# Kernel tuning notes

Measured on AMD Instinct MI355X. Metric: run time of the kernel, lower is better.

The kernel has to match this reference:

```python
import jax, jax.numpy as jnp
import numpy as np

INPUT_DIM = 246
HIDDEN = 512
OUTPUT_DIM = 123
B, T = 128, 500
N_DIFF, N_ABIL = 11, 8


def setup_inputs() -> dict:
    key = jax.random.key(0)
    ks = jax.random.split(key, 9)
    feats = jax.random.normal(ks[0], (B, T, INPUT_DIM), dtype=jnp.float32)
    ability = jax.random.randint(ks[1], (B, T, 1), 0, N_ABIL).astype(jnp.float32)
    diff = jax.random.randint(ks[2], (B, T, 1), 0, N_DIFF).astype(jnp.float32)
    x = jnp.concatenate([feats, ability, diff], axis=-1)  # [B,T,248]
    in_dim = INPUT_DIM + N_DIFF + N_ABIL  # 265
    s_ih = 1.0 / np.sqrt(HIDDEN)
    W_ih = jax.random.uniform(ks[3], (4 * HIDDEN, in_dim), jnp.float32, -s_ih, s_ih)
    W_hh = jax.random.uniform(ks[4], (4 * HIDDEN, HIDDEN), jnp.float32, -s_ih, s_ih)
    b_ih = jax.random.uniform(ks[5], (4 * HIDDEN,), jnp.float32, -s_ih, s_ih)
    b_hh = jax.random.uniform(ks[6], (4 * HIDDEN,), jnp.float32, -s_ih, s_ih)
    s_fc = 1.0 / np.sqrt(HIDDEN)
    W_fc = jax.random.uniform(ks[7], (OUTPUT_DIM, HIDDEN), jnp.float32, -s_fc, s_fc)
    b_fc = jax.random.uniform(ks[8], (OUTPUT_DIM,), jnp.float32, -s_fc, s_fc)
    return {"x": x, "W_ih": W_ih, "W_hh": W_hh, "b_ih": b_ih, "b_hh": b_hh,
            "W_fc": W_fc, "b_fc": b_fc}


def _lstm(x, W_ih, W_hh, b_ih, b_hh):
    # x: [B,T,In] -> out: [B,T,H]; PyTorch gate order i,f,g,o
    Bsz = x.shape[0]
    H = W_hh.shape[1]
    x_proj = jnp.einsum('bti,gi->btg', x, W_ih) + b_ih + b_hh  # [B,T,4H]

    def step(carry, xt):
        h, c = carry
        gates = xt + h @ W_hh.T
        i, f, g, o = jnp.split(gates, 4, axis=-1)
        i, f, o = jax.nn.sigmoid(i), jax.nn.sigmoid(f), jax.nn.sigmoid(o)
        g = jnp.tanh(g)
        c = f * c + i * g
        h = o * jnp.tanh(c)
        return (h, c), h

    h0 = jnp.zeros((Bsz, H), x.dtype)
    c0 = jnp.zeros((Bsz, H), x.dtype)
    (_, _), hs = jax.lax.scan(step, (h0, c0), x_proj.transpose(1, 0, 2))
    return hs.transpose(1, 0, 2)


def reference(x, W_ih, W_hh, b_ih, b_hh, W_fc, b_fc):
    feats = x[..., :INPUT_DIM]
    ability = x[..., -2].astype(jnp.int32)
    diff = x[..., -1].astype(jnp.int32)
    one_hot_diff = jax.nn.one_hot(diff, N_DIFF, dtype=x.dtype)
    one_hot_ab = jax.nn.one_hot(ability, N_ABIL, dtype=x.dtype)
    new_x = jnp.tanh(jnp.concatenate([feats, one_hot_diff, one_hot_ab], axis=-1))
    out = _lstm(new_x, W_ih, W_hh, b_ih, b_hh)  # [B,T,H]
    res = jax.nn.sigmoid(jnp.einsum('bth,oh->bto', out, W_fc) + b_fc)
    return res[:, :-1, :]
```

## Files before the change

kernel.cpp:

```cpp
#include <hip/hip_runtime.h>
#include <hip/hip_fp16.h>


typedef _Float16 f16;
typedef _Float16 f16x8 __attribute__((ext_vector_type(8)));
typedef float f32x4 __attribute__((ext_vector_type(4)));
typedef unsigned u32x4 __attribute__((ext_vector_type(4)));

#define TS 499

#define NEWX_OFF   0ul
#define NEWX_BYTES (500ul*8*9216)
#define HALL_OFF   (NEWX_OFF + NEWX_BYTES)
#define HALL_BYTES (500ul*128*512*2)
#define WHH_OFF    (HALL_OFF + HALL_BYTES)
#define WHH_BYTES  (2048ul*512*2)
#define WIH_OFF    (WHH_OFF + WHH_BYTES)
#define WIH_BYTES  (2048ul*288*2)
#define WFC_OFF    (WIH_OFF + WIH_BYTES)
#define WFC_BYTES  (128ul*512*2)
#define BIAS_OFF   (WFC_OFF + WFC_BYTES)
#define BIAS_BYTES (2048ul*4)
#define WS_NEED    (BIAS_OFF + BIAS_BYTES)

__device__ __forceinline__ float tanh_dev(float x) {
    float ax = fabsf(x);
    float e  = __expf(-2.f * ax);
    float r  = (1.f - e) / (1.f + e);
    return copysignf(r, x);
}
__device__ __forceinline__ float sigm_dev(float x) {
    float e = __expf(-fabsf(x));
    float p = 1.f / (1.f + e);
    return x >= 0.f ? p : 1.f - p;
}

__global__ void __launch_bounds__(256) prep_newx(const float* __restrict__ x,
                                                 f16* __restrict__ newx) {
    const int t  = blockIdx.x;
    const int bt = blockIdx.y;
    const int tid = threadIdx.x;
    char* tb = (char*)newx + ((size_t)t * 8 + bt) * 9216;
    for (int idx = tid; idx < 16 * 288; idx += 256) {
        const int r = idx / 288, k = idx - r * 288;
        const float* xr = x + ((size_t)(bt * 16 + r) * 500 + t) * 248;
        float v;
        if (k < 246)      v = tanh_dev(xr[k]);
        else if (k < 257) v = (k - 246 == (int)xr[247]) ? 0.76159415595576485f : 0.f;
        else if (k < 265) v = (k - 257 == (int)xr[246]) ? 0.76159415595576485f : 0.f;
        else              v = 0.f;
        const int col8 = k >> 3;
        const int byte = (col8 >> 2) * 1024 + (((col8 & 3) * 16 + r) << 4) + ((k & 7) << 1);
        *(f16*)(tb + byte) = (f16)v;
    }
}

__global__ void __launch_bounds__(256) prep_w(const float* __restrict__ W_ih,
                                              const float* __restrict__ W_hh,
                                              const float* __restrict__ W_fc,
                                              const float* __restrict__ b_ih,
                                              const float* __restrict__ b_hh,
                                              f16* __restrict__ whh, f16* __restrict__ wih,
                                              f16* __restrict__ wfc, float* __restrict__ bias) {
    const int NHH = 2048 * 512;
    const int NIH = 2048 * 288;
    const int NFC = 128 * 512;
    const int NT  = NHH + NIH + NFC + 2048;
    for (int i = blockIdx.x * 256 + threadIdx.x; i < NT; i += gridDim.x * 256) {
        if (i < NHH) {
            whh[i] = (f16)W_hh[i];
        } else if (i < NHH + NIH) {
            int j2 = i - NHH; int rr = j2 / 288, kk = j2 % 288;
            wih[j2] = (kk < 265) ? (f16)W_ih[rr * 265 + kk] : (f16)0.f;
        } else if (i < NHH + NIH + NFC) {
            int j2 = i - (NHH + NIH); int rr = j2 >> 9, kk = j2 & 511;
            wfc[j2] = (rr < 123) ? (f16)W_fc[rr * 512 + kk] : (f16)0.f;
        } else {
            int j2 = i - (NHH + NIH + NFC);
            bias[j2] = b_ih[j2] + b_hh[j2];
        }
    }
}

#define CHKU16(H) { u32x4 _u = __builtin_bit_cast(u32x4, H);                  \
    bad |= (unsigned)((_u[0] >> 16) == 0xFFFFu) | (unsigned)((_u[0] & 0xFFFFu) == 0xFFFFu); \
    bad |= (unsigned)((_u[1] >> 16) == 0xFFFFu) | (unsigned)((_u[1] & 0xFFFFu) == 0xFFFFu); \
    bad |= (unsigned)((_u[2] >> 16) == 0xFFFFu) | (unsigned)((_u[2] & 0xFFFFu) == 0xFFFFu); \
    bad |= (unsigned)((_u[3] >> 16) == 0xFFFFu) | (unsigned)((_u[3] & 0xFFFFu) == 0xFFFFu); }

__device__ __forceinline__ u32x4 scrub(u32x4 h) {
    u32x4 u = h;
    #pragma unroll
    for (int i = 0; i < 4; ++i) {
        unsigned v = u[i];
        if ((v & 0xFFFFu) == 0xFFFFu) v &= 0xFFFF0000u;
        if ((v >> 16)     == 0xFFFFu) v &= 0x0000FFFFu;
        u[i] = v;
    }
    return u;
}

__global__ void __launch_bounds__(512, 1) lstm_seq(const f16* __restrict__ newx_,
                                                   f16* __restrict__ hall,
                                                   const f16* __restrict__ whh,
                                                   const f16* __restrict__ wih,
                                                   const float* __restrict__ bias) {
    __shared__ __align__(16) char hsb[16 * 1024];
    __shared__ float gf[4 * 560];
    __shared__ __align__(16) f16 hout[512];

    const char* newx = (const char*)newx_;
    const int tid = threadIdx.x, bid = blockIdx.x;
    const int btile = bid & 7;
    const int hsl   = bid >> 3;

    const int w = tid >> 6, wl = tid & 63;
    const int arow = wl & 15, kgrp = wl >> 4;
    const int g = w & 3, cb = w >> 2;
    const int grow = g * 512 + hsl * 32 + cb * 16 + arow;
    const int bE = tid >> 5, colE = tid & 31;

    f16x8 wh[16], wi[9];
    #pragma unroll
    for (int kc = 0; kc < 16; ++kc)
        wh[kc] = *(const f16x8*)(whh + (size_t)grow * 512 + kc * 32 + kgrp * 8);
    #pragma unroll
    for (int kc = 0; kc < 9; ++kc)
        wi[kc] = *(const f16x8*)(wih + (size_t)grow * 288 + kc * 32 + kgrp * 8);
    const float bb = bias[grow];

    const int srow = tid & 15, sc8 = tid >> 4;
    const int soff1 = (sc8 >> 2) * 1024 + (((sc8 & 3) * 16 + srow) << 4);
    const int soff2 = soff1 + 8 * 1024;

    float c_st = 0.f;

    f16x8 xa[9];
    {
        const char* xt = newx + (size_t)btile * 9216;
        #pragma unroll
        for (int kc = 0; kc < 9; ++kc)
            xa[kc] = *(const f16x8*)(xt + kc * 1024 + wl * 16);
    }

    for (int t = 0; t < TS; ++t) {
        f32x4 acc = {bb, bb, bb, bb};
        #pragma unroll
        for (int kc = 0; kc < 9; ++kc)
            acc = __builtin_amdgcn_mfma_f32_16x16x32_f16(xa[kc], wi[kc], acc, 0, 0, 0);
        {
            const char* xt1 = newx + ((size_t)(t + 1) * 8 + btile) * 9216;
            #pragma unroll
            for (int kc = 0; kc < 9; ++kc)
                xa[kc] = *(const f16x8*)(xt1 + kc * 1024 + wl * 16);
        }

        if (t > 0) {
            const char* hb = (const char*)hall + ((size_t)(t - 1) * 128 + btile * 16) * 1024;
            const char* ga1 = hb + srow * 1024 + sc8 * 16;
            const char* ga2 = ga1 + 512;
            u32x4 h0, h1;
            int spins = 0;
            bool timeout = false;
            for (;;) {
                asm volatile("global_load_dwordx4 %0, %2, off sc0 sc1\n\t"
                             "global_load_dwordx4 %1, %3, off sc0 sc1\n\t"
                             "s_waitcnt vmcnt(0)"
                             : "=&v"(h0), "=&v"(h1) : "v"(ga1), "v"(ga2) : "memory");
                unsigned bad = 0;
                CHKU16(h0); CHKU16(h1);
                if (__ballot(bad) == 0ull) break;
                if (++spins > 4096) { timeout = true; break; }
                if (spins > 2) __builtin_amdgcn_s_sleep(4);
            }
            if (timeout) { h0 = scrub(h0); h1 = scrub(h1); }
            *(u32x4*)(hsb + soff1) = h0;
            *(u32x4*)(hsb + soff2) = h1;
            __syncthreads();

            f32x4 e0 = {0.f,0.f,0.f,0.f}, e1 = {0.f,0.f,0.f,0.f};
            #pragma unroll
            for (int kc = 0; kc < 16; kc += 2) {
                f16x8 a0 = *(const f16x8*)(hsb + kc * 1024 + wl * 16);
                f16x8 a1 = *(const f16x8*)(hsb + (kc + 1) * 1024 + wl * 16);
                e0 = __builtin_amdgcn_mfma_f32_16x16x32_f16(a0, wh[kc],     e0, 0, 0, 0);
                e1 = __builtin_amdgcn_mfma_f32_16x16x32_f16(a1, wh[kc + 1], e1, 0, 0, 0);
            }
            acc += e0; acc += e1;
        }

        {
            float* gp = gf + g * 560 + cb * 16 + (wl & 15);
            const int b4 = (wl >> 4) * 4;
            gp[(b4 + 0) * 35] = acc[0];
            gp[(b4 + 1) * 35] = acc[1];
            gp[(b4 + 2) * 35] = acc[2];
            gp[(b4 + 3) * 35] = acc[3];
        }
        __syncthreads();

        {
            const float* gq = gf + bE * 35 + colE;
            float iv = sigm_dev(gq[0]);
            float fv = sigm_dev(gq[560]);
            float gv = tanh_dev(gq[1120]);
            float ov = sigm_dev(gq[1680]);
            c_st = fv * c_st + iv * gv;
            float hv = ov * tanh_dev(c_st);
            hout[bE * 32 + colE] = (f16)hv;
        }
        __syncthreads();

        if ((tid >> 6) == (t & 7)) {
            u32x4 hv4 = *(const u32x4*)((const char*)hout + wl * 16);
            const f16* sp = hall + ((size_t)t * 128 + btile * 16 + (wl >> 2)) * 512
                            + hsl * 32 + (wl & 3) * 8;
            asm volatile("global_store_dwordx4 %0, %1, off sc0 sc1"
                         :: "v"(sp), "v"(hv4) : "memory");
        }
    }
}

__global__ void __launch_bounds__(256) out_gemm(const f16* __restrict__ hall,
                                                const f16* __restrict__ wfc,
                                                const float* __restrict__ bfc,
                                                float* __restrict__ out) {
    const int tid = threadIdx.x;
    const int w = tid >> 6, wl = tid & 63;
    const int arow = wl & 15, kgrp = wl >> 4;
    const long m0 = (long)blockIdx.x * 64 + w * 16;
    const f16* ap = hall + (m0 + arow) * 512 + kgrp * 8;
    f16x8 a[16];
    #pragma unroll
    for (int kc = 0; kc < 16; ++kc) a[kc] = *(const f16x8*)(ap + kc * 32);
    #pragma unroll
    for (int jt = 0; jt < 8; ++jt) {
        f32x4 acc = {0.f, 0.f, 0.f, 0.f};
        const f16* bp = wfc + (size_t)(jt * 16 + arow) * 512 + kgrp * 8;
        #pragma unroll
        for (int kc = 0; kc < 16; ++kc)
            acc = __builtin_amdgcn_mfma_f32_16x16x32_f16(a[kc], *(const f16x8*)(bp + kc * 32),
                                                         acc, 0, 0, 0);
        const int col = jt * 16 + arow;
        if (col < 123) {
            const float bv = bfc[col];
            #pragma unroll
            for (int rr = 0; rr < 4; ++rr) {
                long m = m0 + kgrp * 4 + rr;
                int tt = (int)(m >> 7), b = (int)(m & 127);
                out[((size_t)b * 499 + tt) * 123 + col] = sigm_dev(acc[rr] + bv);
            }
        }
    }
}

extern "C" void kernel_launch(void* const* d_in, const int* in_sizes, int n_in,
                              void* d_out, int out_size, void* d_ws, size_t ws_size,
                              hipStream_t stream) {
    if (ws_size < WS_NEED) return;

    const float* x    = (const float*)d_in[0];
    const float* W_ih = (const float*)d_in[1];
    const float* W_hh = (const float*)d_in[2];
    const float* b_ih = (const float*)d_in[3];
    const float* b_hh = (const float*)d_in[4];
    const float* W_fc = (const float*)d_in[5];
    const float* b_fc = (const float*)d_in[6];
    float* out = (float*)d_out;
    char* ws = (char*)d_ws;

    f16* newx   = (f16*)(ws + NEWX_OFF);
    f16* hall   = (f16*)(ws + HALL_OFF);
    f16* whh    = (f16*)(ws + WHH_OFF);
    f16* wih    = (f16*)(ws + WIH_OFF);
    f16* wfc    = (f16*)(ws + WFC_OFF);
    float* bias = (float*)(ws + BIAS_OFF);

    (void)hipMemsetAsync(hall, 0xFF, HALL_BYTES, stream);

    prep_newx<<<dim3(TS, 8), 256, 0, stream>>>(x, newx);
    prep_w<<<512, 256, 0, stream>>>(W_ih, W_hh, W_fc, b_ih, b_hh, whh, wih, wfc, bias);

    lstm_seq<<<dim3(128), dim3(512), 0, stream>>>(newx, hall, whh, wih, bias);

    out_gemm<<<998, 256, 0, stream>>>(hall, wfc, b_fc, out);
}
```

Measured before the change: 1.260 ms.

## Give each wave all four gates so the LSTM cell update stays in registers

The persistent LSTM kernel now runs 64 blocks of 256 threads instead of 128 blocks of 512. Each wave computes the i, f, g and o gates for its own 16 hidden columns, so the cell update runs directly on the MFMA accumulators. This drops the shared-memory gate exchange and one barrier per step, and fewer blocks take part in the cross-block spin-wait on h. In exchange each wave does four times the recurrent MFMA work and holds 64 fragments of W_hh in registers. W_ih is no longer kept in registers and is re-read from global memory every step, which adds load latency on the serial critical path.

```diff
diff --git a/kernel.cpp b/kernel.cpp
--- a/kernel.cpp
+++ b/kernel.cpp
@@ -100,40 +100,45 @@
     return u;
 }
 
-__global__ void __launch_bounds__(512, 1) lstm_seq(const f16* __restrict__ newx_,
+#define MFMA16(A, B, C) __builtin_amdgcn_mfma_f32_16x16x32_f16(A, B, C, 0, 0, 0)
+
+__global__ void __launch_bounds__(256, 1) lstm_seq(const f16* __restrict__ newx_,
                                                    f16* __restrict__ hall,
                                                    const f16* __restrict__ whh,
                                                    const f16* __restrict__ wih,
                                                    const float* __restrict__ bias) {
     __shared__ __align__(16) char hsb[16 * 1024];
-    __shared__ float gf[4 * 560];
-    __shared__ __align__(16) f16 hout[512];
+    __shared__ __align__(16) f16 tw[4 * 16 * 16];
 
     const char* newx = (const char*)newx_;
     const int tid = threadIdx.x, bid = blockIdx.x;
     const int btile = bid & 7;
-    const int hsl   = bid >> 3;
+    const int hseg  = bid >> 3;
 
     const int w = tid >> 6, wl = tid & 63;
-    const int arow = wl & 15, kgrp = wl >> 4;
-    const int g = w & 3, cb = w >> 2;
-    const int grow = g * 512 + hsl * 32 + cb * 16 + arow;
-    const int bE = tid >> 5, colE = tid & 31;
-
-    f16x8 wh[16], wi[9];
-    #pragma unroll
-    for (int kc = 0; kc < 16; ++kc)
-        wh[kc] = *(const f16x8*)(whh + (size_t)grow * 512 + kc * 32 + kgrp * 8);
-    #pragma unroll
-    for (int kc = 0; kc < 9; ++kc)
-        wi[kc] = *(const f16x8*)(wih + (size_t)grow * 288 + kc * 32 + kgrp * 8);
-    const float bb = bias[grow];
-
-    const int srow = tid & 15, sc8 = tid >> 4;
-    const int soff1 = (sc8 >> 2) * 1024 + (((sc8 & 3) * 16 + srow) << 4);
-    const int soff2 = soff1 + 8 * 1024;
-
-    float c_st = 0.f;
+    const int col = wl & 15, kgrp = wl >> 4;
+    const int c0 = hseg * 64 + w * 16;
+    const int r0 = kgrp * 4;
+
+    f16x8 wh0[16], wh1[16], wh2[16], wh3[16];
+    {
+        const size_t rb = (size_t)(c0 + col) * 512 + kgrp * 8;
+        #pragma unroll
+        for (int kc = 0; kc < 16; ++kc) {
+            wh0[kc] = *(const f16x8*)(whh + rb                + kc * 32);
+            wh1[kc] = *(const f16x8*)(whh + rb + 512ul * 512  + kc * 32);
+            wh2[kc] = *(const f16x8*)(whh + rb + 1024ul * 512 + kc * 32);
+            wh3[kc] = *(const f16x8*)(whh + rb + 1536ul * 512 + kc * 32);
+        }
+    }
+    const float b_i = bias[c0 + col],        b_f = bias[512 + c0 + col];
+    const float b_g = bias[1024 + c0 + col], b_o = bias[1536 + c0 + col];
+    const f16* const wib = wih + (size_t)(c0 + col) * 288 + kgrp * 8;
+
+    const int srow = tid & 15, sc = tid >> 4;
+    const int soff0 = (sc >> 2) * 1024 + (((sc & 3) * 16 + srow) << 4);
+
+    f32x4 c_st = {0.f, 0.f, 0.f, 0.f};
 
     f16x8 xa[9];
     {
@@ -144,10 +149,55 @@
     }
 
     for (int t = 0; t < TS; ++t) {
-        f32x4 acc = {bb, bb, bb, bb};
-        #pragma unroll
-        for (int kc = 0; kc < 9; ++kc)
-            acc = __builtin_amdgcn_mfma_f32_16x16x32_f16(xa[kc], wi[kc], acc, 0, 0, 0);
+        if (t > 0) {
+            const char* gb = (const char*)hall + ((size_t)(t - 1) * 128 + btile * 16) * 1024
+                             + srow * 1024 + sc * 16;
+            u32x4 h0, h1, h2, h3;
+            int spins = 0;
+            bool timeout = false;
+            for (;;) {
+                asm volatile(
+                    "global_load_dwordx4 %0, %4, off sc0 sc1\n\t"
+                    "global_load_dwordx4 %1, %4, off offset:256 sc0 sc1\n\t"
+                    "global_load_dwordx4 %2, %4, off offset:512 sc0 sc1\n\t"
+                    "global_load_dwordx4 %3, %4, off offset:768 sc0 sc1\n\t"
+                    "s_waitcnt vmcnt(0)"
+                    : "=&v"(h0), "=&v"(h1), "=&v"(h2), "=&v"(h3)
+                    : "v"(gb) : "memory");
+                unsigned bad = 0;
+                CHKU16(h0); CHKU16(h1); CHKU16(h2); CHKU16(h3);
+                if (__ballot(bad) == 0ull) break;
+                if (++spins > 4096) { timeout = true; break; }
+                if (spins > 2) __builtin_amdgcn_s_sleep(4);
+            }
+            if (timeout) { h0 = scrub(h0); h1 = scrub(h1); h2 = scrub(h2); h3 = scrub(h3); }
+            *(u32x4*)(hsb + soff0)         = h0;
+            *(u32x4*)(hsb + soff0 + 4096)  = h1;
+            *(u32x4*)(hsb + soff0 + 8192)  = h2;
+            *(u32x4*)(hsb + soff0 + 12288) = h3;
+        }
+        __syncthreads();
+
+        f32x4 ai = {b_i, b_i, b_i, b_i}, af = {b_f, b_f, b_f, b_f};
+        f32x4 ag = {b_g, b_g, b_g, b_g}, ao = {b_o, b_o, b_o, b_o};
+        if (t > 0) {
+            #pragma unroll
+            for (int kc = 0; kc < 16; ++kc) {
+                f16x8 a = *(const f16x8*)(hsb + kc * 1024 + wl * 16);
+                ai = MFMA16(a, wh0[kc], ai);
+                af = MFMA16(a, wh1[kc], af);
+                ag = MFMA16(a, wh2[kc], ag);
+                ao = MFMA16(a, wh3[kc], ao);
+            }
+        }
+        #pragma unroll
+        for (int kc = 0; kc < 9; ++kc) {
+            f16x8 a = xa[kc];
+            ai = MFMA16(a, *(const f16x8*)(wib                 + kc * 32), ai);
+            af = MFMA16(a, *(const f16x8*)(wib + 512ul * 288   + kc * 32), af);
+            ag = MFMA16(a, *(const f16x8*)(wib + 1024ul * 288  + kc * 32), ag);
+            ao = MFMA16(a, *(const f16x8*)(wib + 1536ul * 288  + kc * 32), ao);
+        }
         {
             const char* xt1 = newx + ((size_t)(t + 1) * 8 + btile) * 9216;
             #pragma unroll
@@ -155,66 +205,24 @@
                 xa[kc] = *(const f16x8*)(xt1 + kc * 1024 + wl * 16);
         }
 
-        if (t > 0) {
-            const char* hb = (const char*)hall + ((size_t)(t - 1) * 128 + btile * 16) * 1024;
-            const char* ga1 = hb + srow * 1024 + sc8 * 16;
-            const char* ga2 = ga1 + 512;
-            u32x4 h0, h1;
-            int spins = 0;
-            bool timeout = false;
-            for (;;) {
-                asm volatile("global_load_dwordx4 %0, %2, off sc0 sc1\n\t"
-                             "global_load_dwordx4 %1, %3, off sc0 sc1\n\t"
-                             "s_waitcnt vmcnt(0)"
-                             : "=&v"(h0), "=&v"(h1) : "v"(ga1), "v"(ga2) : "memory");
-                unsigned bad = 0;
-                CHKU16(h0); CHKU16(h1);
-                if (__ballot(bad) == 0ull) break;
-                if (++spins > 4096) { timeout = true; break; }
-                if (spins > 2) __builtin_amdgcn_s_sleep(4);
-            }
-            if (timeout) { h0 = scrub(h0); h1 = scrub(h1); }
-            *(u32x4*)(hsb + soff1) = h0;
-            *(u32x4*)(hsb + soff2) = h1;
-            __syncthreads();
-
-            f32x4 e0 = {0.f,0.f,0.f,0.f}, e1 = {0.f,0.f,0.f,0.f};
-            #pragma unroll
-            for (int kc = 0; kc < 16; kc += 2) {
-                f16x8 a0 = *(const f16x8*)(hsb + kc * 1024 + wl * 16);
-                f16x8 a1 = *(const f16x8*)(hsb + (kc + 1) * 1024 + wl * 16);
-                e0 = __builtin_amdgcn_mfma_f32_16x16x32_f16(a0, wh[kc],     e0, 0, 0, 0);
-                e1 = __builtin_amdgcn_mfma_f32_16x16x32_f16(a1, wh[kc + 1], e1, 0, 0, 0);
-            }
-            acc += e0; acc += e1;
-        }
-
-        {
-            float* gp = gf + g * 560 + cb * 16 + (wl & 15);
-            const int b4 = (wl >> 4) * 4;
-            gp[(b4 + 0) * 35] = acc[0];
-            gp[(b4 + 1) * 35] = acc[1];
-            gp[(b4 + 2) * 35] = acc[2];
-            gp[(b4 + 3) * 35] = acc[3];
+        #pragma unroll
+        for (int i = 0; i < 4; ++i) {
+            float iv = sigm_dev(ai[i]);
+            float fv = sigm_dev(af[i]);
+            float gv = tanh_dev(ag[i]);
+            float ov = sigm_dev(ao[i]);
+            c_st[i] = fv * c_st[i] + iv * gv;
+            float hv = ov * tanh_dev(c_st[i]);
+            tw[w * 256 + (r0 + i) * 16 + col] = (f16)hv;
         }
         __syncthreads();
 
-        {
-            const float* gq = gf + bE * 35 + colE;
-            float iv = sigm_dev(gq[0]);
-            float fv = sigm_dev(gq[560]);
-            float gv = tanh_dev(gq[1120]);
-            float ov = sigm_dev(gq[1680]);
-            c_st = fv * c_st + iv * gv;
-            float hv = ov * tanh_dev(c_st);
-            hout[bE * 32 + colE] = (f16)hv;
-        }
-        __syncthreads();
-
-        if ((tid >> 6) == (t & 7)) {
-            u32x4 hv4 = *(const u32x4*)((const char*)hout + wl * 16);
-            const f16* sp = hall + ((size_t)t * 128 + btile * 16 + (wl >> 2)) * 512
-                            + hsl * 32 + (wl & 3) * 8;
+        if (tid < 128) {
+            const int r = tid >> 3, cu = tid & 7;
+            u32x4 hv4 = *(const u32x4*)((const char*)tw + (cu >> 1) * 512 + r * 32
+                                        + (cu & 1) * 16);
+            const f16* sp = hall + ((size_t)t * 128 + btile * 16 + r) * 512
+                            + hseg * 64 + cu * 8;
             asm volatile("global_store_dwordx4 %0, %1, off sc0 sc1"
                          :: "v"(sp), "v"(hv4) : "memory");
         }
@@ -281,7 +289,7 @@
     prep_newx<<<dim3(TS, 8), 256, 0, stream>>>(x, newx);
     prep_w<<<512, 256, 0, stream>>>(W_ih, W_hh, W_fc, b_ih, b_hh, whh, wih, wfc, bias);
 
-    lstm_seq<<<dim3(128), dim3(512), 0, stream>>>(newx, hall, whh, wih, bias);
+    lstm_seq<<<dim3(64), dim3(256), 0, stream>>>(newx, hall, whh, wih, bias);
 
     out_gemm<<<998, 256, 0, stream>>>(hall, wfc, b_fc, out);
 }
```

After: 2.918 ms. 2.32x slower.
